# Performance work log

Measured on AMD Instinct MI355X. Metric: run time of the kernel, lower is better.

## Reference

```python
import jax, jax.numpy as jnp
import numpy as np
from jax import lax

B, D, H = 128, 256, 8
DK = D // H


def hollow_mask():
    # Chess-move-shaped 15x15 sparsity mask (1 = keep weight, 0 = zero)
    m = np.ones((15, 15), np.float32)
    for c in range(5):
        m[1 + c:7, c] = 0; m[8:14 - c, c] = 0
        m[c, 1 + c:7] = 0; m[c, 8:14 - c] = 0
        m[1 + c:7, 14 - c] = 0; m[8:14 - c, 14 - c] = 0
        m[14 - c, 1 + c:7] = 0; m[14 - c, 8:14 - c] = 0
    return m


def setup_inputs() -> dict:
    key = jax.random.key(0)
    ks = jax.random.split(key, 12)
    mask = jnp.asarray(hollow_mask())[None, None]  # [1,1,15,15]
    fan = 1.0 / np.sqrt(D * 15 * 15)
    def conv_w(k):
        return jax.random.uniform(k, (D, D, 15, 15), jnp.float32, -fan, fan) * mask
    def conv_b(k):
        return jax.random.uniform(k, (D,), jnp.float32, -fan, fan)
    lin_fan = 1.0 / np.sqrt(D)
    return {
        "q": jax.random.normal(ks[0], (B, 8, 8, D), jnp.float32),
        "k": jax.random.normal(ks[1], (B, 8, 8, D), jnp.float32),
        "v": jax.random.normal(ks[2], (B, 8, 8, D), jnp.float32),
        "wk": conv_w(ks[3]), "bk": conv_b(ks[4]),
        "wq": conv_w(ks[5]), "bq": conv_b(ks[6]),
        "wv": conv_w(ks[7]), "bv": conv_b(ks[8]),
        "wo": jax.random.uniform(ks[9], (D, D), jnp.float32, -lin_fan, lin_fan),
        "bo": jax.random.uniform(ks[10], (D,), jnp.float32, -lin_fan, lin_fan),
    }


def _conv(x, w, b):
    # x: [B,D,8,8], w: [D,D,15,15] (OIHW), padding 7 -> same 8x8 output
    y = lax.conv_general_dilated(x, w, (1, 1), [(7, 7), (7, 7)],
                                 dimension_numbers=("NCHW", "OIHW", "NCHW"))
    return y + b[None, :, None, None]


def _branch(x, w1, b1, w2, b2):
    # permute to NCHW, conv -> relu -> conv, back to [B,64,H,DK]
    x = jnp.transpose(x, (0, 3, 1, 2))            # [B,D,8,8]
    x = jax.nn.relu(_conv(x, w1, b1))
    x = _conv(x, w2, b2)
    x = jnp.transpose(x, (0, 2, 3, 1)).reshape(x.shape[0], 64, H, DK)
    return jnp.transpose(x, (0, 2, 1, 3))         # [B,H,64,DK]


def reference(q, k, v, wk, bk, wq, bq, wv, bv, wo, bo):
    bsz = q.shape[0]
    # NOTE: faithful to the torch code — k and q branches both use k_conv for
    # the SECOND conv; v branch uses v_conv twice.
    kh = _branch(k, wk, bk, wk, bk)
    qh = _branch(q, wq, bq, wk, bk)
    vh = _branch(v, wv, bv, wv, bv)
    scores = jnp.einsum("bhqd,bhkd->bhqk", qh, kh) / np.sqrt(DK)
    attn = jax.nn.softmax(scores, axis=-1)        # [B,H,64,64]
    out = jnp.einsum("bhqk,bhkd->bhqd", attn, vh)  # [B,H,64,DK]
    concat = jnp.transpose(out, (0, 2, 1, 3)).reshape(bsz, 64, D)
    out = concat @ wo.T + bo                       # torch Linear
    return out.reshape(bsz, 8, 8, D)
```

## Files before the change

kernel.cpp:

```cpp
#include <hip/hip_runtime.h>
#include <hip/hip_bf16.h>

#define DEV __device__ __forceinline__

typedef float  f32x4  __attribute__((ext_vector_type(4)));
typedef __bf16 bf16x8 __attribute__((ext_vector_type(8)));

DEV unsigned short f2b(float x){
  union { float f; unsigned u; } v; v.f = x;
  unsigned r = v.u + 0x7FFFu + ((v.u >> 16) & 1u);
  return (unsigned short)(r >> 16);
}
DEV float b2f(unsigned short h){
  union { unsigned u; float f; } v; v.u = ((unsigned)h) << 16;
  return v.f;
}

struct CMap { short m[225]; };
constexpr CMap make_cmap(){
  CMap c{};
  int n = 0;
  for (int t = 0; t < 225; ++t){
    int r = t / 15, cc = t % 15;
    int rp = r < 14 - r ? r : 14 - r;
    int cp = cc < 14 - cc ? cc : 14 - cc;
    bool z = (cp <= 4 && rp >= cp + 1 && rp <= 6) || (rp <= 4 && cp >= rp + 1 && cp <= 6);
    c.m[t] = z ? (short)-1 : (short)(n++);
  }
  return c;
}
__constant__ CMap CMAP = make_cmap();

#define GLDS(gp, lp) __builtin_amdgcn_global_load_lds( \
    (const __attribute__((address_space(1))) void*)(const void*)(gp), \
    (__attribute__((address_space(3))) void*)(void*)(lp), 16, 0, 0)

__global__ __launch_bounds__(256) void pack_w_k(
    const float* __restrict__ w0, const float* __restrict__ w1,
    const float* __restrict__ w2, unsigned short* __restrict__ Wp){
  __shared__ unsigned short sw[65][258];
  const int widx = blockIdx.x >> 8;
  const int o    = blockIdx.x & 255;
  const float4* src = (const float4*)((widx == 0 ? w0 : (widx == 1 ? w1 : w2)) + (size_t)o * 57600);
  unsigned short* dst = Wp + (size_t)widx * 65 * 65536 + (size_t)o * 256;
  for (int idx4 = threadIdx.x; idx4 < 14400; idx4 += 256){
    float4 val = src[idx4];
    int e = idx4 * 4;
    float vv[4] = {val.x, val.y, val.z, val.w};
#pragma unroll
    for (int j = 0; j < 4; ++j){
      int ee = e + j;
      int i = ee / 225;
      int t = ee - i * 225;
      short c = CMAP.m[t];
      if (c >= 0) sw[c][i] = f2b(vv[j]);
    }
  }
  __syncthreads();
  for (int idx = threadIdx.x; idx < 65 * 128; idx += 256){
    int t = idx >> 7, i2 = idx & 127;
    *(ushort2*)(dst + (size_t)t * 65536 + i2 * 2) = *(const ushort2*)&sw[t][i2 * 2];
  }
}

__global__ void pack_wo_k(const float4* __restrict__ wo, ushort4* __restrict__ WO){
  int i = blockIdx.x * 256 + threadIdx.x;
  float4 a = wo[i];
  WO[i] = make_ushort4(f2b(a.x), f2b(a.y), f2b(a.z), f2b(a.w));
}

__global__ void prep_k(const float4* __restrict__ q, const float4* __restrict__ k,
                       const float4* __restrict__ v, ushort4* __restrict__ xq,
                       ushort4* __restrict__ xk, ushort4* __restrict__ xv){
  int i = blockIdx.x * 256 + threadIdx.x;
  float4 a = q[i]; xq[i] = make_ushort4(f2b(a.x), f2b(a.y), f2b(a.z), f2b(a.w));
  a = k[i];        xk[i] = make_ushort4(f2b(a.x), f2b(a.y), f2b(a.z), f2b(a.w));
  a = v[i];        xv[i] = make_ushort4(f2b(a.x), f2b(a.y), f2b(a.z), f2b(a.w));
}

template<bool RELU>
__global__ __launch_bounds__(256, 3) void conv_mm(
    const unsigned short* __restrict__ X0, const unsigned short* __restrict__ X1,
    const unsigned short* __restrict__ X2,
    const unsigned short* __restrict__ W0, const unsigned short* __restrict__ W1,
    const unsigned short* __restrict__ W2,
    const float* __restrict__ bias0, const float* __restrict__ bias1,
    const float* __restrict__ bias2,
    unsigned short* __restrict__ Yo0, unsigned short* __restrict__ Yo1,
    unsigned short* __restrict__ Yo2)
{
  __shared__ unsigned short lA[2][64 * 64];
  __shared__ unsigned short lB[2][128 * 64];
  __shared__ int   qtap[64];
  __shared__ int   nq_sh;

  const int L   = blockIdx.x + 64 * blockIdx.y + 128 * blockIdx.z;
  const int swz = (L & 7) * 96 + (L >> 3);
  const int p     = swz & 63;
  const int o0    = ((swz >> 6) & 1) * 128;
  const int zz    = swz >> 7;
  const int br    = zz >> 1;
  const int brow0 = (zz & 1) * 64;
  const unsigned short* X    = br == 0 ? X0 : (br == 1 ? X1 : X2);
  const unsigned short* W    = br == 0 ? W0 : (br == 1 ? W1 : W2);
  const float*          bias = br == 0 ? bias0 : (br == 1 ? bias1 : bias2);
  unsigned short*       Y    = br == 0 ? Yo0 : (br == 1 ? Yo1 : Yo2);

  const int tid = threadIdx.x;
  if (tid == 0){
    int py = p >> 3, px = p & 7, m = 0;
    for (int q = 0; q < 64; ++q){
      int qy = q >> 3, qx = q & 7;
      int t = (7 + qy - py) * 15 + (7 + qx - px);
      short c = CMAP.m[t];
      if (c >= 0) qtap[m++] = (q << 8) | (int)c;
    }
    nq_sh = m;
  }
  __syncthreads();
  const int nq     = nq_sh;
  const int nsteps = nq * 4;

  const int wv_ = tid >> 6, ln = tid & 63;
  const int lr = ln & 15, lk = ln >> 4;
  const int wm = wv_ >> 1, wn = wv_ & 1;
  f32x4 acc[2][4] = {};

  auto stage = [&](int buf, int s){
    int e   = qtap[s >> 2];
    int kkc = (s & 3) * 64;
    int q   = e >> 8, tap = e & 255;
    int r = ln >> 3, c = ln & 7;
#pragma unroll
    for (int r2 = 0; r2 < 2; ++r2){
      int rowb = r2 * 32 + wv_ * 8;
      int row  = rowb + r;
      int csw  = c ^ (row & 7);
      GLDS(X + (size_t)(brow0 + row) * 16384 + q * 256 + kkc + csw * 8, &lA[buf][rowb * 64]);
    }
#pragma unroll
    for (int r2 = 0; r2 < 4; ++r2){
      int rowb = r2 * 32 + wv_ * 8;
      int row  = rowb + r;
      int csw  = c ^ (row & 7);
      GLDS(W + (size_t)tap * 65536 + (size_t)(o0 + row) * 256 + kkc + csw * 8, &lB[buf][rowb * 64]);
    }
  };

  stage(0, 0);
  for (int s = 0; s < nsteps; ++s){
    int buf = s & 1;
    if (s + 1 < nsteps){
      stage(buf ^ 1, s + 1);
      asm volatile("s_waitcnt vmcnt(6)" ::: "memory");
    } else {
      asm volatile("s_waitcnt vmcnt(0)" ::: "memory");
    }
    __builtin_amdgcn_sched_barrier(0);
    __builtin_amdgcn_s_barrier();
#pragma unroll
    for (int ks = 0; ks < 2; ++ks){
      bf16x8 a[2], bb[4];
      int cb = ks * 4 + lk;
#pragma unroll
      for (int mm = 0; mm < 2; ++mm){
        int row = wm * 32 + mm * 16 + lr;
        a[mm] = *(const bf16x8*)&lA[buf][row * 64 + ((cb ^ (row & 7)) << 3)];
      }
#pragma unroll
      for (int nn = 0; nn < 4; ++nn){
        int row = wn * 64 + nn * 16 + lr;
        bb[nn] = *(const bf16x8*)&lB[buf][row * 64 + ((cb ^ (row & 7)) << 3)];
      }
#pragma unroll
      for (int mm = 0; mm < 2; ++mm)
#pragma unroll
        for (int nn = 0; nn < 4; ++nn)
          acc[mm][nn] = __builtin_amdgcn_mfma_f32_16x16x32_bf16(a[mm], bb[nn], acc[mm][nn], 0, 0, 0);
    }
    __builtin_amdgcn_s_barrier();
  }

#pragma unroll
  for (int mm = 0; mm < 2; ++mm)
#pragma unroll
    for (int nn = 0; nn < 4; ++nn)
#pragma unroll
      for (int rr = 0; rr < 4; ++rr){
        int row = wm * 32 + mm * 16 + lk * 4 + rr;
        int col = wn * 64 + nn * 16 + lr;
        int b = brow0 + row, o = o0 + col;
        float val = acc[mm][nn][rr] + bias[o];
        if (RELU) val = fmaxf(val, 0.f);
        Y[(size_t)(b * 64 + p) * 256 + o] = f2b(val);
      }
}

__global__ __launch_bounds__(256) void attn_k(
    const unsigned short* __restrict__ Yq, const unsigned short* __restrict__ Yk,
    const unsigned short* __restrict__ Yv, unsigned short* __restrict__ CC)
{
  __shared__ float qs[64][33], ksh[64][33], vs[64][33];
  __shared__ float sc[64][65];
  const int b = blockIdx.x >> 3, h = blockIdx.x & 7;
  const size_t base = (size_t)b * 16384 + h * 32;
  for (int idx = threadIdx.x; idx < 2048; idx += 256){
    int pq = idx >> 5, dk = idx & 31;
    size_t g = base + (size_t)pq * 256 + dk;
    qs[pq][dk]  = b2f(Yq[g]);
    ksh[pq][dk] = b2f(Yk[g]);
    vs[pq][dk]  = b2f(Yv[g]);
  }
  __syncthreads();
  {
    int r = threadIdx.x >> 2, qd = threadIdx.x & 3;
    float qv[32];
#pragma unroll
    for (int d = 0; d < 32; ++d) qv[d] = qs[r][d];
    for (int j = 0; j < 16; ++j){
      int pk = qd * 16 + j;
      float a = 0.f;
#pragma unroll
      for (int d = 0; d < 32; ++d) a += qv[d] * ksh[pk][d];
      sc[r][pk] = a * 0.17677669529663687f;
    }
  }
  __syncthreads();
  if (threadIdx.x < 64){
    int r = threadIdx.x;
    float m = -1e30f;
    for (int j = 0; j < 64; ++j) m = fmaxf(m, sc[r][j]);
    float ssum = 0.f;
    for (int j = 0; j < 64; ++j){ float e = __expf(sc[r][j] - m); sc[r][j] = e; ssum += e; }
    float inv = 1.f / ssum;
    for (int j = 0; j < 64; ++j) sc[r][j] *= inv;
  }
  __syncthreads();
  for (int idx = threadIdx.x; idx < 2048; idx += 256){
    int pq = idx >> 5, dk = idx & 31;
    float a = 0.f;
#pragma unroll
    for (int pk = 0; pk < 64; ++pk) a += sc[pq][pk] * vs[pk][dk];
    CC[base + (size_t)pq * 256 + dk] = f2b(a);
  }
}

__global__ __launch_bounds__(256, 3) void fin_mm(
    const unsigned short* __restrict__ A, const unsigned short* __restrict__ Bw,
    const float* __restrict__ bo, float* __restrict__ out)
{
  __shared__ unsigned short lA[2][64 * 64];
  __shared__ unsigned short lB[2][128 * 64];
  const int m0 = blockIdx.x * 64;
  const int o0 = blockIdx.y * 128;
  const int tid = threadIdx.x;
  const int wv_ = tid >> 6, ln = tid & 63;
  const int lr = ln & 15, lk = ln >> 4;
  const int wm = wv_ >> 1, wn = wv_ & 1;
  f32x4 acc[2][4] = {};

  auto stage = [&](int buf, int s){
    int kkc = s * 64;
    int r = ln >> 3, c = ln & 7;
#pragma unroll
    for (int r2 = 0; r2 < 2; ++r2){
      int rowb = r2 * 32 + wv_ * 8;
      int row  = rowb + r;
      int csw  = c ^ (row & 7);
      GLDS(A + (size_t)(m0 + row) * 256 + kkc + csw * 8, &lA[buf][rowb * 64]);
    }
#pragma unroll
    for (int r2 = 0; r2 < 4; ++r2){
      int rowb = r2 * 32 + wv_ * 8;
      int row  = rowb + r;
      int csw  = c ^ (row & 7);
      GLDS(Bw + (size_t)(o0 + row) * 256 + kkc + csw * 8, &lB[buf][rowb * 64]);
    }
  };

  stage(0, 0);
  for (int s = 0; s < 4; ++s){
    int buf = s & 1;
    if (s < 3){
      stage(buf ^ 1, s + 1);
      asm volatile("s_waitcnt vmcnt(6)" ::: "memory");
    } else {
      asm volatile("s_waitcnt vmcnt(0)" ::: "memory");
    }
    __builtin_amdgcn_sched_barrier(0);
    __builtin_amdgcn_s_barrier();
#pragma unroll
    for (int ks = 0; ks < 2; ++ks){
      bf16x8 a[2], bb[4];
      int cb = ks * 4 + lk;
#pragma unroll
      for (int mm = 0; mm < 2; ++mm){
        int row = wm * 32 + mm * 16 + lr;
        a[mm] = *(const bf16x8*)&lA[buf][row * 64 + ((cb ^ (row & 7)) << 3)];
      }
#pragma unroll
      for (int nn = 0; nn < 4; ++nn){
        int row = wn * 64 + nn * 16 + lr;
        bb[nn] = *(const bf16x8*)&lB[buf][row * 64 + ((cb ^ (row & 7)) << 3)];
      }
#pragma unroll
      for (int mm = 0; mm < 2; ++mm)
#pragma unroll
        for (int nn = 0; nn < 4; ++nn)
          acc[mm][nn] = __builtin_amdgcn_mfma_f32_16x16x32_bf16(a[mm], bb[nn], acc[mm][nn], 0, 0, 0);
    }
    __builtin_amdgcn_s_barrier();
  }

#pragma unroll
  for (int mm = 0; mm < 2; ++mm)
#pragma unroll
    for (int nn = 0; nn < 4; ++nn)
#pragma unroll
      for (int rr = 0; rr < 4; ++rr){
        int row = wm * 32 + mm * 16 + lk * 4 + rr;
        int col = wn * 64 + nn * 16 + lr;
        out[(size_t)(m0 + row) * 256 + o0 + col] = acc[mm][nn][rr] + bo[o0 + col];
      }
}

extern "C" void kernel_launch(void* const* d_in, const int* in_sizes, int n_in,
                              void* d_out, int out_size, void* d_ws, size_t ws_size,
                              hipStream_t stream){
  const float* q  = (const float*)d_in[0];
  const float* k  = (const float*)d_in[1];
  const float* v  = (const float*)d_in[2];
  const float* wk = (const float*)d_in[3];
  const float* bk = (const float*)d_in[4];
  const float* wq = (const float*)d_in[5];
  const float* bq = (const float*)d_in[6];
  const float* wv = (const float*)d_in[7];
  const float* bv = (const float*)d_in[8];
  const float* wo = (const float*)d_in[9];
  const float* bo = (const float*)d_in[10];
  float* out = (float*)d_out;

  constexpr size_t WPS = 65ull * 65536;
  constexpr size_t XSZ = 2097152ull;

  char* ws = (char*)d_ws;
  size_t off = 0;
  auto alloc = [&](size_t bytes){ void* p = ws + off; off += (bytes + 255) & ~(size_t)255; return p; };
  unsigned short* Wp  = (unsigned short*)alloc(3 * WPS * 2);
  unsigned short* WO  = (unsigned short*)alloc(65536 * 2);
  unsigned short* Xq  = (unsigned short*)alloc(XSZ * 2);
  unsigned short* Xk  = (unsigned short*)alloc(XSZ * 2);
  unsigned short* Xv  = (unsigned short*)alloc(XSZ * 2);
  unsigned short* Y1q = (unsigned short*)alloc(XSZ * 2);
  unsigned short* Y1k = (unsigned short*)alloc(XSZ * 2);
  unsigned short* Y1v = (unsigned short*)alloc(XSZ * 2);
  unsigned short* Y2q = (unsigned short*)alloc(XSZ * 2);
  unsigned short* Y2k = (unsigned short*)alloc(XSZ * 2);
  unsigned short* Y2v = (unsigned short*)alloc(XSZ * 2);
  unsigned short* CC  = (unsigned short*)alloc(XSZ * 2);
  (void)ws_size; (void)in_sizes; (void)n_in; (void)out_size;

  pack_w_k<<<dim3(768), 256, 0, stream>>>(wq, wk, wv, Wp);
  pack_wo_k<<<dim3(64), 256, 0, stream>>>((const float4*)wo, (ushort4*)WO);
  prep_k<<<dim3(2048), 256, 0, stream>>>((const float4*)q, (const float4*)k, (const float4*)v,
                                         (ushort4*)Xq, (ushort4*)Xk, (ushort4*)Xv);
  conv_mm<true><<<dim3(64, 2, 6), 256, 0, stream>>>(
      Xq, Xk, Xv, Wp, Wp + WPS, Wp + 2 * WPS, bq, bk, bv, Y1q, Y1k, Y1v);
  conv_mm<false><<<dim3(64, 2, 6), 256, 0, stream>>>(
      Y1q, Y1k, Y1v, Wp + WPS, Wp + WPS, Wp + 2 * WPS, bk, bk, bv, Y2q, Y2k, Y2v);
  attn_k<<<dim3(1024), 256, 0, stream>>>(Y2q, Y2k, Y2v, CC);
  fin_mm<<<dim3(128, 2), 256, 0, stream>>>(CC, WO, bo, out);
}
```

Before: 607.7 us.

## Split-K across wave pairs in conv_mm and reorder pixels by tap count

Each wave now computes a full 64x64 tile but only on alternate pipeline steps: wave pair kp handles odd or even K-steps, and the partial sums are reduced through LDS at the end. This doubles per-wave accumulators, halving MFMA work per wave per step while each wave reuses more A/B fragments. A constexpr longest-processing-time permutation maps blocks to output pixels so that pixels with more active taps are scheduled first, reducing tail imbalance. Risks: higher register pressure from 64 accumulator floats at launch_bounds(256,3), idle waves on each step so per-step latency may not shrink, and an extra LDS reduction epilogue.

```diff
diff --git a/kernel.cpp b/kernel.cpp
--- a/kernel.cpp
+++ b/kernel.cpp
@@ -30,6 +30,30 @@
   return c;
 }
 __constant__ CMap CMAP = make_cmap();
+
+struct Perm { unsigned char v[64]; };
+constexpr Perm make_lpt(){
+  CMap cm = make_cmap();
+  int nq[64] = {};
+  for (int p = 0; p < 64; ++p){
+    int py = p >> 3, px = p & 7, n = 0;
+    for (int q = 0; q < 64; ++q){
+      int qy = q >> 3, qx = q & 7;
+      if (cm.m[(7 + qy - py) * 15 + (7 + qx - px)] >= 0) n++;
+    }
+    nq[p] = n;
+  }
+  Perm pr{};
+  bool used[64] = {};
+  for (int i = 0; i < 64; ++i){
+    int best = 0, bv = -1;
+    for (int p = 0; p < 64; ++p) if (!used[p] && nq[p] > bv){ bv = nq[p]; best = p; }
+    used[best] = true;
+    pr.v[i] = (unsigned char)best;
+  }
+  return pr;
+}
+__constant__ Perm LPT = make_lpt();
 
 #define GLDS(gp, lp) __builtin_amdgcn_global_load_lds( \
     (const __attribute__((address_space(1))) void*)(const void*)(gp), \
@@ -89,14 +113,13 @@
     unsigned short* __restrict__ Yo0, unsigned short* __restrict__ Yo1,
     unsigned short* __restrict__ Yo2)
 {
-  __shared__ unsigned short lA[2][64 * 64];
-  __shared__ unsigned short lB[2][128 * 64];
-  __shared__ int   qtap[64];
-  __shared__ int   nq_sh;
+  __shared__ unsigned short lds[24576];
+  __shared__ int qtap[64];
+  __shared__ int nq_sh;
 
   const int L   = blockIdx.x + 64 * blockIdx.y + 128 * blockIdx.z;
   const int swz = (L & 7) * 96 + (L >> 3);
-  const int p     = swz & 63;
+  const int p     = LPT.v[swz & 63];
   const int o0    = ((swz >> 6) & 1) * 128;
   const int zz    = swz >> 7;
   const int br    = zz >> 1;
@@ -123,27 +146,30 @@
 
   const int wv_ = tid >> 6, ln = tid & 63;
   const int lr = ln & 15, lk = ln >> 4;
-  const int wm = wv_ >> 1, wn = wv_ & 1;
-  f32x4 acc[2][4] = {};
+  const int wn = wv_ & 1;
+  const int kp = wv_ >> 1;
+  f32x4 acc[4][4] = {};
 
   auto stage = [&](int buf, int s){
     int e   = qtap[s >> 2];
     int kkc = (s & 3) * 64;
     int q   = e >> 8, tap = e & 255;
     int r = ln >> 3, c = ln & 7;
+    unsigned short* lA = lds + buf * 4096;
+    unsigned short* lB = lds + 8192 + buf * 8192;
 #pragma unroll
     for (int r2 = 0; r2 < 2; ++r2){
       int rowb = r2 * 32 + wv_ * 8;
       int row  = rowb + r;
       int csw  = c ^ (row & 7);
-      GLDS(X + (size_t)(brow0 + row) * 16384 + q * 256 + kkc + csw * 8, &lA[buf][rowb * 64]);
+      GLDS(X + (size_t)(brow0 + row) * 16384 + q * 256 + kkc + csw * 8, lA + rowb * 64);
     }
 #pragma unroll
     for (int r2 = 0; r2 < 4; ++r2){
       int rowb = r2 * 32 + wv_ * 8;
       int row  = rowb + r;
       int csw  = c ^ (row & 7);
-      GLDS(W + (size_t)tap * 65536 + (size_t)(o0 + row) * 256 + kkc + csw * 8, &lB[buf][rowb * 64]);
+      GLDS(W + (size_t)tap * 65536 + (size_t)(o0 + row) * 256 + kkc + csw * 8, lB + rowb * 64);
     }
   };
 
@@ -158,42 +184,63 @@
     }
     __builtin_amdgcn_sched_barrier(0);
     __builtin_amdgcn_s_barrier();
-#pragma unroll
-    for (int ks = 0; ks < 2; ++ks){
-      bf16x8 a[2], bb[4];
-      int cb = ks * 4 + lk;
-#pragma unroll
-      for (int mm = 0; mm < 2; ++mm){
-        int row = wm * 32 + mm * 16 + lr;
-        a[mm] = *(const bf16x8*)&lA[buf][row * 64 + ((cb ^ (row & 7)) << 3)];
+    if ((s & 1) == kp){
+      const unsigned short* lAb = lds + buf * 4096;
+      const unsigned short* lBb = lds + 8192 + buf * 8192;
+#pragma unroll
+      for (int ks = 0; ks < 2; ++ks){
+        bf16x8 a[4], bb[4];
+        int cb = ks * 4 + lk;
+#pragma unroll
+        for (int mm = 0; mm < 4; ++mm){
+          int row = mm * 16 + lr;
+          a[mm] = *(const bf16x8*)&lAb[row * 64 + ((cb ^ (row & 7)) << 3)];
+        }
+#pragma unroll
+        for (int nn = 0; nn < 4; ++nn){
+          int row = wn * 64 + nn * 16 + lr;
+          bb[nn] = *(const bf16x8*)&lBb[row * 64 + ((cb ^ (row & 7)) << 3)];
+        }
+#pragma unroll
+        for (int mm = 0; mm < 4; ++mm)
+#pragma unroll
+          for (int nn = 0; nn < 4; ++nn)
+            acc[mm][nn] = __builtin_amdgcn_mfma_f32_16x16x32_bf16(a[mm], bb[nn], acc[mm][nn], 0, 0, 0);
       }
-#pragma unroll
-      for (int nn = 0; nn < 4; ++nn){
-        int row = wn * 64 + nn * 16 + lr;
-        bb[nn] = *(const bf16x8*)&lB[buf][row * 64 + ((cb ^ (row & 7)) << 3)];
-      }
-#pragma unroll
-      for (int mm = 0; mm < 2; ++mm)
-#pragma unroll
-        for (int nn = 0; nn < 4; ++nn)
-          acc[mm][nn] = __builtin_amdgcn_mfma_f32_16x16x32_bf16(a[mm], bb[nn], acc[mm][nn], 0, 0, 0);
     }
     __builtin_amdgcn_s_barrier();
   }
 
-#pragma unroll
-  for (int mm = 0; mm < 2; ++mm)
-#pragma unroll
-    for (int nn = 0; nn < 4; ++nn)
-#pragma unroll
-      for (int rr = 0; rr < 4; ++rr){
-        int row = wm * 32 + mm * 16 + lk * 4 + rr;
-        int col = wn * 64 + nn * 16 + lr;
-        int b = brow0 + row, o = o0 + col;
-        float val = acc[mm][nn][rr] + bias[o];
-        if (RELU) val = fmaxf(val, 0.f);
-        Y[(size_t)(b * 64 + p) * 256 + o] = f2b(val);
-      }
+  __syncthreads();
+  float* scr = (float*)lds;
+  if (kp == 1){
+#pragma unroll
+    for (int mm = 0; mm < 4; ++mm)
+#pragma unroll
+      for (int nn = 0; nn < 4; ++nn)
+#pragma unroll
+        for (int rr = 0; rr < 4; ++rr){
+          int row = mm * 16 + lk * 4 + rr;
+          int col = nn * 16 + lr;
+          scr[wn * 4096 + row * 64 + col] = acc[mm][nn][rr];
+        }
+  }
+  __syncthreads();
+  if (kp == 0){
+#pragma unroll
+    for (int mm = 0; mm < 4; ++mm)
+#pragma unroll
+      for (int nn = 0; nn < 4; ++nn)
+#pragma unroll
+        for (int rr = 0; rr < 4; ++rr){
+          int row = mm * 16 + lk * 4 + rr;
+          int col = nn * 16 + lr;
+          int b = brow0 + row, o = o0 + wn * 64 + col;
+          float val = acc[mm][nn][rr] + scr[wn * 4096 + row * 64 + col] + bias[o];
+          if (RELU) val = fmaxf(val, 0.f);
+          Y[(size_t)(b * 64 + p) * 256 + o] = f2b(val);
+        }
+  }
 }
 
 __global__ __launch_bounds__(256) void attn_k(
```

Result: slower. 622.7 us (+2.5%).
